# Optimization experiments

Hardware: AMD Instinct MI355X
Metric: run time of the kernel (lower is better)

## Reference

```python
import jax, jax.numpy as jnp
import numpy as np

IN_FEATURES = 4096
OUT_FEATURES = 11008
B, S = 8, 512


def setup_inputs() -> dict:
    key = jax.random.key(0)
    k1, k2, k3 = jax.random.split(key, 3)
    x = jax.random.normal(k1, (B, S, IN_FEATURES), dtype=jnp.float32)
    # int8 weights simulated as int32 values in [-127, 127]
    weight_int8 = jax.random.randint(k2, (OUT_FEATURES, IN_FEATURES), -127, 128, dtype=jnp.int32)
    # per-output-channel scales (positive, small, like absmax/127)
    weight_scale = jax.random.uniform(k3, (OUT_FEATURES,), dtype=jnp.float32) * 0.01 + 1e-4
    return {"x": x, "weight_int8": weight_int8, "weight_scale": weight_scale}


def reference(x, weight_int8, weight_scale):
    # On-the-fly dequantization: W[o, i] = int8[o, i] * scale[o]
    weight = weight_int8.astype(x.dtype) * weight_scale.astype(x.dtype)[:, None]
    # F.linear: y = x @ W^T  -> [B, S, out_features]
    return jnp.einsum('bsi,oi->bso', x, weight)
```

## Files before the change

kernel.cpp:

```cpp
#include <hip/hip_runtime.h>
#include <stdint.h>

#define M_DIM 4096
#define N_DIM 11008
#define K_DIM 4096

typedef int i32x4 __attribute__((ext_vector_type(4)));

static __device__ __forceinline__ void direct_load16(const void* gptr, void* ldsptr) {
    __builtin_amdgcn_global_load_lds(
        (const __attribute__((address_space(1))) void*)gptr,
        (__attribute__((address_space(3))) void*)ldsptr,
        16, 0, 0);
}

__global__ __launch_bounds__(256) void cvt_w_kernel(const int* __restrict__ w,
                                                    int8_t* __restrict__ o) {
    int t = blockIdx.x * 256 + threadIdx.x;
    const int4* w4 = (const int4*)w;
    int4 a = w4[t];
    ((unsigned*)o)[t] = (a.x & 255) | ((a.y & 255) << 8) | ((a.z & 255) << 16) | (a.w << 24);
}

__global__ __launch_bounds__(256) void quant_x_kernel(const float* __restrict__ x,
                                                      int8_t* __restrict__ xq,
                                                      float* __restrict__ xs) {
    __shared__ float wmax[4];
    const int row = blockIdx.x;
    const int t = threadIdx.x;
    const float4* xr = (const float4*)(x + (size_t)row * K_DIM);

    float4 v[4];
    float am = 0.0f;
#pragma unroll
    for (int p = 0; p < 4; p++) {
        v[p] = xr[p * 256 + t];
        am = fmaxf(am, fmaxf(fmaxf(fabsf(v[p].x), fabsf(v[p].y)),
                             fmaxf(fabsf(v[p].z), fabsf(v[p].w))));
    }
#pragma unroll
    for (int o = 32; o > 0; o >>= 1)
        am = fmaxf(am, __shfl_xor(am, o));
    if ((t & 63) == 0) wmax[t >> 6] = am;
    __syncthreads();
    am = fmaxf(fmaxf(wmax[0], wmax[1]), fmaxf(wmax[2], wmax[3]));

    const float inv = 127.0f / am;
    int* oq = (int*)(xq + (size_t)row * K_DIM);
#pragma unroll
    for (int p = 0; p < 4; p++) {
        int qa = (int)rintf(v[p].x * inv);
        int qb = (int)rintf(v[p].y * inv);
        int qc = (int)rintf(v[p].z * inv);
        int qd = (int)rintf(v[p].w * inv);
        oq[p * 256 + t] = (qa & 255) | ((qb & 255) << 8) | ((qc & 255) << 16) | (qd << 24);
    }
    if (t == 0) xs[row] = am * (1.0f / 127.0f);
}


__global__ __launch_bounds__(512, 2) void gemm_i8_kernel(
    const int8_t* __restrict__ A,
    const int8_t* __restrict__ B,
    const float* __restrict__ xs,
    const float* __restrict__ ws,
    float* __restrict__ C)
{
    __shared__ __align__(16) int8_t As[4][256 * 64];
    __shared__ __align__(16) int8_t Bs[4][256 * 64];

    const int tid  = threadIdx.x;
    const int lane = tid & 63;
    const int wave = tid >> 6;
    const int wm   = wave >> 2;
    const int wn   = wave & 3;
    const int quad = lane >> 4;
    const int r16  = lane & 15;

    const int orig = blockIdx.x + (blockIdx.y << 4);
    const int work = (orig & 7) * 86 + (orig >> 3);
    const int m0 = (work & 15) * 256;
    const int n0 = (work >> 4) * 256;

    const int srow   = tid >> 2;
    const int schunk = (tid & 3) ^ ((tid >> 3) & 3);
    const int8_t* gA = A + (size_t)(m0 + srow) * K_DIM + schunk * 16;
    const int8_t* gB = B + (size_t)(n0 + srow) * K_DIM + schunk * 16;
    const size_t half2 = (size_t)128 * K_DIM;
    const int wb = wave * 1024;

    const int fsw   = (r16 >> 1) & 3;
    const int a_off = (wm * 128 + r16) * 64 + ((quad ^ fsw) * 16);
    const int b_off = (wn * 64  + r16) * 64 + ((quad ^ fsw) * 16);

    i32x4 acc[8][4];
#pragma unroll
    for (int i = 0; i < 8; i++)
#pragma unroll
        for (int j = 0; j < 4; j++) acc[i][j] = (i32x4)(0);

#define STAGE_A(t, buf) do {                                                  \
        direct_load16(gA + (size_t)(t) * 64,         (char*)As[buf] + wb);    \
        direct_load16(gA + (size_t)(t) * 64 + half2, (char*)As[buf] + wb + 8192); \
    } while (0)
#define STAGE_B(t, buf) do {                                                  \
        direct_load16(gB + (size_t)(t) * 64,         (char*)Bs[buf] + wb);    \
        direct_load16(gB + (size_t)(t) * 64 + half2, (char*)Bs[buf] + wb + 8192); \
    } while (0)

    STAGE_A(0, 0); STAGE_B(0, 0);
    STAGE_A(1, 1); STAGE_B(1, 1);
    STAGE_A(2, 2); STAGE_B(2, 2);
    asm volatile("s_waitcnt vmcnt(8)" ::: "memory");
    __builtin_amdgcn_s_barrier();

    for (int t = 0; t < 64; ++t) {
        const int b  = t & 3;
        const int sb = (t + 3) & 3;
        const int s  = (t + 3 > 63) ? 63 : t + 3;

        const int8_t* as = As[b];
        const int8_t* bs = Bs[b];
        i32x4 bf[4];
#pragma unroll
        for (int j = 0; j < 4; j++)
            bf[j] = *(const i32x4*)(bs + b_off + j * 1024);
        i32x4 af[8];
#pragma unroll
        for (int i = 0; i < 8; i++)
            af[i] = *(const i32x4*)(as + a_off + i * 1024);

        STAGE_A(s, sb);
        STAGE_B(s, sb);

        __builtin_amdgcn_s_setprio(1);
#pragma unroll
        for (int i = 0; i < 8; i++)
#pragma unroll
            for (int j = 0; j < 4; j++)
                acc[i][j] = __builtin_amdgcn_mfma_i32_16x16x64_i8(
                    af[i], bf[j], acc[i][j], 0, 0, 0);
        __builtin_amdgcn_s_setprio(0);

        asm volatile("s_waitcnt vmcnt(8)" ::: "memory");
        __builtin_amdgcn_s_barrier();
    }

#undef STAGE_B
#undef STAGE_A

#pragma unroll
    for (int i = 0; i < 8; i++) {
        const int mrow = m0 + wm * 128 + i * 16 + quad * 4;
        float rsc[4];
#pragma unroll
        for (int r = 0; r < 4; r++) rsc[r] = xs[mrow + r];
#pragma unroll
        for (int j = 0; j < 4; j++) {
            const int n = n0 + wn * 64 + j * 16 + r16;
            const float sc = ws[n];
#pragma unroll
            for (int r = 0; r < 4; r++)
                C[(size_t)(mrow + r) * N_DIM + n] = (float)acc[i][j][r] * sc * rsc[r];
        }
    }
}


extern "C" void kernel_launch(void* const* d_in, const int* in_sizes, int n_in,
                              void* d_out, int out_size, void* d_ws, size_t ws_size,
                              hipStream_t stream) {
    const float* x       = (const float*)d_in[0];
    const int*   w_int   = (const int*)d_in[1];
    const float* w_scale = (const float*)d_in[2];
    float*       out     = (float*)d_out;

    int8_t* wq = (int8_t*)d_ws;
    int8_t* xq = (int8_t*)((char*)d_ws + (size_t)N_DIM * K_DIM);
    float*  xs = (float*)((char*)d_ws + (size_t)N_DIM * K_DIM + (size_t)M_DIM * K_DIM);

    cvt_w_kernel<<<dim3(N_DIM * K_DIM / 4 / 256), dim3(256), 0, stream>>>(w_int, wq);
    quant_x_kernel<<<dim3(M_DIM), dim3(256), 0, stream>>>(x, xq, xs);
    gemm_i8_kernel<<<dim3(M_DIM / 256, N_DIM / 256), dim3(512), 0, stream>>>(xq, wq, xs, w_scale, out);
}
```

Measured before the change: 545.3 us.

## Load A fragments directly from global in MFMA-native layout, bypassing LDS

The activation quantizer now writes int8 x in a layout that matches the MFMA fragments, so each lane of the GEMM can read its A fragments straight from global memory into registers with coalesced 16-byte loads. The LDS space previously used for A tiles is given to B, which now uses an 8-deep LDS ring with a 4-stage lookahead. The mapping from block index to tile is also changed. The intent is to remove LDS traffic and LDS reads for A. The cost is that global-memory latency for A now sits directly in the loop: a single vmcnt wait covers both the A register loads and the B LDS copies, so that latency may be exposed every iteration.

```diff
diff --git a/kernel.cpp b/kernel.cpp
--- a/kernel.cpp
+++ b/kernel.cpp
@@ -46,14 +46,19 @@
     am = fmaxf(fmaxf(wmax[0], wmax[1]), fmaxf(wmax[2], wmax[3]));
 
     const float inv = 127.0f / am;
-    int* oq = (int*)(xq + (size_t)row * K_DIM);
+    int* oq = (int*)xq;
+    const int mt = row >> 4, ml = row & 15;
 #pragma unroll
     for (int p = 0; p < 4; p++) {
         int qa = (int)rintf(v[p].x * inv);
         int qb = (int)rintf(v[p].y * inv);
         int qc = (int)rintf(v[p].z * inv);
         int qd = (int)rintf(v[p].w * inv);
-        oq[p * 256 + t] = (qa & 255) | ((qb & 255) << 8) | ((qc & 255) << 16) | (qd << 24);
+        const int packed = (qa & 255) | ((qb & 255) << 8) | ((qc & 255) << 16) | (qd << 24);
+        const int w0 = p * 256 + t;
+        const int idx = (((mt << 6) + (w0 >> 4)) << 8)
+                      + (((((w0 >> 2) & 3) << 4) | ml) << 2) + (w0 & 3);
+        oq[idx] = packed;
     }
     if (t == 0) xs[row] = am * (1.0f / 127.0f);
 }
@@ -66,8 +71,7 @@
     const float* __restrict__ ws,
     float* __restrict__ C)
 {
-    __shared__ __align__(16) int8_t As[4][256 * 64];
-    __shared__ __align__(16) int8_t Bs[4][256 * 64];
+    __shared__ __align__(16) int8_t Bs[8][256 * 64];
 
     const int tid  = threadIdx.x;
     const int lane = tid & 63;
@@ -77,21 +81,24 @@
     const int quad = lane >> 4;
     const int r16  = lane & 15;
 
-    const int orig = blockIdx.x + (blockIdx.y << 4);
-    const int work = (orig & 7) * 86 + (orig >> 3);
-    const int m0 = (work & 15) * 256;
-    const int n0 = (work >> 4) * 256;
+    const int orig  = blockIdx.x + (blockIdx.y << 4);
+    const int ix    = orig >> 3;
+    const int hi    = (ix >= 43) ? 1 : 0;
+    const int m_idx = ((orig & 7) << 1) + hi;
+    const int n_idx = ix - hi * 43;
+    const int m0 = m_idx * 256;
+    const int n0 = n_idx * 256;
 
     const int srow   = tid >> 2;
     const int schunk = (tid & 3) ^ ((tid >> 3) & 3);
-    const int8_t* gA = A + (size_t)(m0 + srow) * K_DIM + schunk * 16;
     const int8_t* gB = B + (size_t)(n0 + srow) * K_DIM + schunk * 16;
     const size_t half2 = (size_t)128 * K_DIM;
     const int wb = wave * 1024;
 
     const int fsw   = (r16 >> 1) & 3;
-    const int a_off = (wm * 128 + r16) * 64 + ((quad ^ fsw) * 16);
-    const int b_off = (wn * 64  + r16) * 64 + ((quad ^ fsw) * 16);
+    const int b_off = (wn * 64 + r16) * 64 + ((quad ^ fsw) * 16);
+
+    const int8_t* pA = A + ((size_t)(m_idx * 16 + wm * 8)) * 65536 + lane * 16;
 
     i32x4 acc[8][4];
 #pragma unroll
@@ -99,39 +106,29 @@
 #pragma unroll
         for (int j = 0; j < 4; j++) acc[i][j] = (i32x4)(0);
 
-#define STAGE_A(t, buf) do {                                                  \
-        direct_load16(gA + (size_t)(t) * 64,         (char*)As[buf] + wb);    \
-        direct_load16(gA + (size_t)(t) * 64 + half2, (char*)As[buf] + wb + 8192); \
-    } while (0)
+    i32x4 af[8], bf[4];
+
 #define STAGE_B(t, buf) do {                                                  \
         direct_load16(gB + (size_t)(t) * 64,         (char*)Bs[buf] + wb);    \
         direct_load16(gB + (size_t)(t) * 64 + half2, (char*)Bs[buf] + wb + 8192); \
     } while (0)
 
-    STAGE_A(0, 0); STAGE_B(0, 0);
-    STAGE_A(1, 1); STAGE_B(1, 1);
-    STAGE_A(2, 2); STAGE_B(2, 2);
-    asm volatile("s_waitcnt vmcnt(8)" ::: "memory");
-    __builtin_amdgcn_s_barrier();
+    STAGE_B(0, 0); STAGE_B(1, 1); STAGE_B(2, 2); STAGE_B(3, 3);
+#pragma unroll
+    for (int i = 0; i < 8; i++)
+        af[i] = *(const i32x4*)(pA + i * 65536);
 
     for (int t = 0; t < 64; ++t) {
-        const int b  = t & 3;
-        const int sb = (t + 3) & 3;
-        const int s  = (t + 3 > 63) ? 63 : t + 3;
+        const int s = (t + 4 > 63) ? 63 : t + 4;
+        STAGE_B(s, (t + 4) & 7);
 
-        const int8_t* as = As[b];
-        const int8_t* bs = Bs[b];
-        i32x4 bf[4];
+        asm volatile("s_waitcnt vmcnt(4)" ::: "memory");
+        __builtin_amdgcn_s_barrier();
+
+        const int8_t* bs = Bs[t & 7];
 #pragma unroll
         for (int j = 0; j < 4; j++)
             bf[j] = *(const i32x4*)(bs + b_off + j * 1024);
-        i32x4 af[8];
-#pragma unroll
-        for (int i = 0; i < 8; i++)
-            af[i] = *(const i32x4*)(as + a_off + i * 1024);
-
-        STAGE_A(s, sb);
-        STAGE_B(s, sb);
 
         __builtin_amdgcn_s_setprio(1);
 #pragma unroll
@@ -142,12 +139,14 @@
                     af[i], bf[j], acc[i][j], 0, 0, 0);
         __builtin_amdgcn_s_setprio(0);
 
-        asm volatile("s_waitcnt vmcnt(8)" ::: "memory");
-        __builtin_amdgcn_s_barrier();
+        if (t < 63) {
+#pragma unroll
+            for (int i = 0; i < 8; i++)
+                af[i] = *(const i32x4*)(pA + i * 65536 + (size_t)(t + 1) * 1024);
+        }
     }
 
 #undef STAGE_B
-#undef STAGE_A
 
 #pragma unroll
     for (int i = 0; i < 8; i++) {
```

New measurement: 589.4 us. 1.08x slower.
